# Kernel tuning notes

Hardware: AMD Instinct MI355X
Metric: run time of the kernel (lower is better)

The kernel has to match this reference:

```python
import jax, jax.numpy as jnp
import numpy as np

B, K, D = 8192, 256, 128


def setup_inputs() -> dict:
    key = jax.random.key(0)
    k1, k2 = jax.random.split(key)
    z = jax.random.normal(k1, (B, D), dtype=jnp.float32)
    centroids = jax.random.normal(k2, (K, D), dtype=jnp.float32)
    logvar = jnp.zeros((K, D), dtype=jnp.float32)
    return {"z": z, "centroids": centroids, "logvar": logvar}


def reference(z, centroids, logvar):
    # Mahalanobis (diagonal-covariance) distance of each z row to each centroid.
    # dist[b,k] = sum_d (z[b,d] - mu[k,d])^2 / var[k,d]
    diff = z[:, None, :] - centroids[None, :, :]          # (B, K, D)
    var = jnp.exp(logvar)[None, :, :]                      # (1, K, D)
    dist = jnp.sum(diff * diff / var, axis=2)              # (B, K)
    # Soft assignments: softmax over clusters of -0.5 * dist (stable softmax).
    return jax.nn.softmax(-0.5 * dist, axis=1)             # (B, K)
```

## Files before the change

kernel.cpp:

```cpp
#include <hip/hip_runtime.h>


typedef short     bf16x8  __attribute__((ext_vector_type(8)));
typedef float     f32x4   __attribute__((ext_vector_type(4)));
typedef unsigned short ushort_t;
typedef ushort_t  ushort8 __attribute__((ext_vector_type(8)));

constexpr int Bn = 8192, Kn = 256, Dn = 128;

__device__ __forceinline__ ushort_t bf16_rn(float x) {
    unsigned u = __float_as_uint(x);
    u = (u + 0x7FFFu + ((u >> 16) & 1u)) >> 16;
    return (ushort_t)u;
}
__device__ __forceinline__ float bf16f(ushort_t h) {
    return __uint_as_float(((unsigned)h) << 16);
}

__global__ __launch_bounds__(1024, 4)
void gmm_fused(const float* __restrict__ z, const float* __restrict__ cent,
               const float* __restrict__ lvar, float* __restrict__ out)
{
    __shared__ ushort_t Ah[32 * 256];
    __shared__ ushort_t Al[32 * 256];
    __shared__ float red[32][16];

    const int tid = threadIdx.x;
    const int w   = tid >> 6;
    const int l   = tid & 63;
    const int lg  = l >> 4;
    const int ll  = l & 15;
    const int b0  = blockIdx.x * 32;
    const int n0  = w * 16;

    bf16x8 Bh[8], Bl[8];
    float cpart = 0.0f;
    const size_t crow = (size_t)(n0 + ll) * Dn + lg * 4;
    #pragma unroll
    for (int kk = 0; kk < 8; ++kk) {
        const float4 cv = *reinterpret_cast<const float4*>(cent + crow + kk * 16);
        const float4 l4 = *reinterpret_cast<const float4*>(lvar + crow + kk * 16);
        const float a0 = __expf(-l4.x), a1 = __expf(-l4.y);
        const float a2 = __expf(-l4.z), a3 = __expf(-l4.w);
        const float f[8] = {a0, -2.0f * cv.x * a0, a1, -2.0f * cv.y * a1,
                            a2, -2.0f * cv.z * a2, a3, -2.0f * cv.w * a3};
        ushort8 hi8, lo8;
        #pragma unroll
        for (int j = 0; j < 8; ++j) {
            ushort_t h = bf16_rn(f[j]);
            hi8[j] = h;
            lo8[j] = bf16_rn(f[j] - bf16f(h));
        }
        Bh[kk] = (bf16x8)hi8;
        Bl[kk] = (bf16x8)lo8;
        cpart += cv.x * cv.x * a0 + cv.y * cv.y * a1 +
                 cv.z * cv.z * a2 + cv.w * cv.w * a3;
    }
    cpart += __shfl_xor(cpart, 16);
    cpart += __shfl_xor(cpart, 32);
    const float ck = cpart;

    {
        const int row = tid >> 5;
        const int dq  = tid & 31;
        const float4 v = *reinterpret_cast<const float4*>(z + (size_t)(b0 + row) * Dn + dq * 4);
        const float f[8] = {v.x * v.x, v.x, v.y * v.y, v.y,
                            v.z * v.z, v.z, v.w * v.w, v.w};
        ushort8 hi8, lo8;
        #pragma unroll
        for (int j = 0; j < 8; ++j) {
            ushort_t h = bf16_rn(f[j]);
            hi8[j] = h;
            lo8[j] = bf16_rn(f[j] - bf16f(h));
        }
        const int off = (row * 256 + dq * 8) ^ ((row & 7) << 3);
        *reinterpret_cast<ushort8*>(&Ah[off]) = hi8;
        *reinterpret_cast<ushort8*>(&Al[off]) = lo8;
    }
    __syncthreads();

    f32x4 acc0 = (f32x4){0.f, 0.f, 0.f, 0.f};
    f32x4 acc1 = (f32x4){0.f, 0.f, 0.f, 0.f};
    const int ar0 = ll * 256 + lg * 8;
    const int ar1 = ar0 + 16 * 256;
    const int sw  = (ll & 7) << 3;

    #pragma unroll
    for (int kk = 0; kk < 8; ++kk) {
        const int o = kk * 32;
        const bf16x8 a0h = *reinterpret_cast<const bf16x8*>(&Ah[(ar0 + o) ^ sw]);
        const bf16x8 a0l = *reinterpret_cast<const bf16x8*>(&Al[(ar0 + o) ^ sw]);
        const bf16x8 a1h = *reinterpret_cast<const bf16x8*>(&Ah[(ar1 + o) ^ sw]);
        const bf16x8 a1l = *reinterpret_cast<const bf16x8*>(&Al[(ar1 + o) ^ sw]);

        acc0 = __builtin_amdgcn_mfma_f32_16x16x32_bf16(a0h, Bh[kk], acc0, 0, 0, 0);
        acc1 = __builtin_amdgcn_mfma_f32_16x16x32_bf16(a1h, Bh[kk], acc1, 0, 0, 0);
        acc0 = __builtin_amdgcn_mfma_f32_16x16x32_bf16(a0h, Bl[kk], acc0, 0, 0, 0);
        acc1 = __builtin_amdgcn_mfma_f32_16x16x32_bf16(a1h, Bl[kk], acc1, 0, 0, 0);
        acc0 = __builtin_amdgcn_mfma_f32_16x16x32_bf16(a0l, Bh[kk], acc0, 0, 0, 0);
        acc1 = __builtin_amdgcn_mfma_f32_16x16x32_bf16(a1l, Bh[kk], acc1, 0, 0, 0);
    }

    float dv[2][4];
    #pragma unroll
    for (int r = 0; r < 4; ++r) { dv[0][r] = acc0[r] + ck; dv[1][r] = acc1[r] + ck; }

    #pragma unroll
    for (int mi = 0; mi < 2; ++mi)
        #pragma unroll
        for (int r = 0; r < 4; ++r) {
            float t = dv[mi][r];
            t = fminf(t, __shfl_xor(t, 1));
            t = fminf(t, __shfl_xor(t, 2));
            t = fminf(t, __shfl_xor(t, 4));
            t = fminf(t, __shfl_xor(t, 8));
            if (ll == 0) red[mi * 16 + lg * 4 + r][w] = t;
        }
    __syncthreads();

    float gm[2][4];
    #pragma unroll
    for (int mi = 0; mi < 2; ++mi)
        #pragma unroll
        for (int r = 0; r < 4; ++r) {
            const int row = mi * 16 + lg * 4 + r;
            const f32x4* rp = reinterpret_cast<const f32x4*>(&red[row][0]);
            f32x4 m4 = rp[0];
            #pragma unroll
            for (int q = 1; q < 4; ++q) {
                f32x4 v = rp[q];
                m4[0] = fminf(m4[0], v[0]); m4[1] = fminf(m4[1], v[1]);
                m4[2] = fminf(m4[2], v[2]); m4[3] = fminf(m4[3], v[3]);
            }
            gm[mi][r] = fminf(fminf(m4[0], m4[1]), fminf(m4[2], m4[3]));
        }
    __syncthreads();

    float pv[2][4];
    #pragma unroll
    for (int mi = 0; mi < 2; ++mi)
        #pragma unroll
        for (int r = 0; r < 4; ++r) {
            const float p = __expf(-0.5f * (dv[mi][r] - gm[mi][r]));
            pv[mi][r] = p;
            float s = p;
            s += __shfl_xor(s, 1);
            s += __shfl_xor(s, 2);
            s += __shfl_xor(s, 4);
            s += __shfl_xor(s, 8);
            if (ll == 0) red[mi * 16 + lg * 4 + r][w] = s;
        }
    __syncthreads();

    #pragma unroll
    for (int mi = 0; mi < 2; ++mi)
        #pragma unroll
        for (int r = 0; r < 4; ++r) {
            const int row = mi * 16 + lg * 4 + r;
            const f32x4* rp = reinterpret_cast<const f32x4*>(&red[row][0]);
            f32x4 s4 = rp[0];
            #pragma unroll
            for (int q = 1; q < 4; ++q) {
                f32x4 v = rp[q];
                s4[0] += v[0]; s4[1] += v[1]; s4[2] += v[2]; s4[3] += v[3];
            }
            const float inv = 1.0f / ((s4[0] + s4[1]) + (s4[2] + s4[3]));
            out[(size_t)(b0 + row) * Kn + n0 + ll] = pv[mi][r] * inv;
        }
}

extern "C" void kernel_launch(void* const* d_in, const int* in_sizes, int n_in,
                              void* d_out, int out_size, void* d_ws, size_t ws_size,
                              hipStream_t stream) {
    const float* z      = (const float*)d_in[0];
    const float* cent   = (const float*)d_in[1];
    const float* logvar = (const float*)d_in[2];
    float* out = (float*)d_out;
    (void)in_sizes; (void)n_in; (void)out_size; (void)d_ws; (void)ws_size;

    hipLaunchKernelGGL(gmm_fused, dim3(Bn / 32), dim3(1024), 0, stream,
                       z, cent, logvar, out);
}
```

Before: 25.35 us.

## Stream centroid prep into MFMA loop and store A tile in MFMA order

```diff
diff --git a/kernel.cpp b/kernel.cpp
--- a/kernel.cpp
+++ b/kernel.cpp
@@ -1,28 +1,38 @@
 #include <hip/hip_runtime.h>
+#include <hip/hip_bf16.h>
 
 
 typedef short     bf16x8  __attribute__((ext_vector_type(8)));
 typedef float     f32x4   __attribute__((ext_vector_type(4)));
 typedef unsigned short ushort_t;
-typedef ushort_t  ushort8 __attribute__((ext_vector_type(8)));
 
 constexpr int Bn = 8192, Kn = 256, Dn = 128;
 
-__device__ __forceinline__ ushort_t bf16_rn(float x) {
-    unsigned u = __float_as_uint(x);
-    u = (u + 0x7FFFu + ((u >> 16) & 1u)) >> 16;
-    return (ushort_t)u;
+__device__ __forceinline__ short bfbits(__hip_bfloat16 h) {
+    return __builtin_bit_cast(short, h);
 }
-__device__ __forceinline__ float bf16f(ushort_t h) {
-    return __uint_as_float(((unsigned)h) << 16);
+
+__device__ __forceinline__ void split8(const float* f, bf16x8& hi, bf16x8& lo) {
+    #pragma unroll
+    for (int p = 0; p < 4; ++p) {
+        const float2 fp = make_float2(f[2 * p], f[2 * p + 1]);
+        const __hip_bfloat162 h2 = __float22bfloat162_rn(fp);
+        hi[2 * p]     = bfbits(h2.x);
+        hi[2 * p + 1] = bfbits(h2.y);
+        const float2 rp = make_float2(fp.x - __bfloat162float(h2.x),
+                                      fp.y - __bfloat162float(h2.y));
+        const __hip_bfloat162 l2 = __float22bfloat162_rn(rp);
+        lo[2 * p]     = bfbits(l2.x);
+        lo[2 * p + 1] = bfbits(l2.y);
+    }
 }
 
 __global__ __launch_bounds__(1024, 4)
 void gmm_fused(const float* __restrict__ z, const float* __restrict__ cent,
                const float* __restrict__ lvar, float* __restrict__ out)
 {
-    __shared__ ushort_t Ah[32 * 256];
-    __shared__ ushort_t Al[32 * 256];
+    __shared__ ushort_t Ah[2 * 8 * 64 * 8];
+    __shared__ ushort_t Al[2 * 8 * 64 * 8];
     __shared__ float red[32][16];
 
     const int tid = threadIdx.x;
@@ -33,73 +43,65 @@
     const int b0  = blockIdx.x * 32;
     const int n0  = w * 16;
 
-    bf16x8 Bh[8], Bl[8];
-    float cpart = 0.0f;
-    const size_t crow = (size_t)(n0 + ll) * Dn + lg * 4;
-    #pragma unroll
-    for (int kk = 0; kk < 8; ++kk) {
-        const float4 cv = *reinterpret_cast<const float4*>(cent + crow + kk * 16);
-        const float4 l4 = *reinterpret_cast<const float4*>(lvar + crow + kk * 16);
-        const float a0 = __expf(-l4.x), a1 = __expf(-l4.y);
-        const float a2 = __expf(-l4.z), a3 = __expf(-l4.w);
-        const float f[8] = {a0, -2.0f * cv.x * a0, a1, -2.0f * cv.y * a1,
-                            a2, -2.0f * cv.z * a2, a3, -2.0f * cv.w * a3};
-        ushort8 hi8, lo8;
-        #pragma unroll
-        for (int j = 0; j < 8; ++j) {
-            ushort_t h = bf16_rn(f[j]);
-            hi8[j] = h;
-            lo8[j] = bf16_rn(f[j] - bf16f(h));
-        }
-        Bh[kk] = (bf16x8)hi8;
-        Bl[kk] = (bf16x8)lo8;
-        cpart += cv.x * cv.x * a0 + cv.y * cv.y * a1 +
-                 cv.z * cv.z * a2 + cv.w * cv.w * a3;
-    }
-    cpart += __shfl_xor(cpart, 16);
-    cpart += __shfl_xor(cpart, 32);
-    const float ck = cpart;
-
     {
-        const int row = tid >> 5;
-        const int dq  = tid & 31;
-        const float4 v = *reinterpret_cast<const float4*>(z + (size_t)(b0 + row) * Dn + dq * 4);
+        const int r   = tid >> 9;
+        const int kks = (tid >> 6) & 7;
+        const int row = r * 16 + ll;
+        const int d0  = kks * 16 + lg * 4;
+        const float4 v = *reinterpret_cast<const float4*>(
+            z + (size_t)(b0 + row) * Dn + d0);
         const float f[8] = {v.x * v.x, v.x, v.y * v.y, v.y,
                             v.z * v.z, v.z, v.w * v.w, v.w};
-        ushort8 hi8, lo8;
-        #pragma unroll
-        for (int j = 0; j < 8; ++j) {
-            ushort_t h = bf16_rn(f[j]);
-            hi8[j] = h;
-            lo8[j] = bf16_rn(f[j] - bf16f(h));
-        }
-        const int off = (row * 256 + dq * 8) ^ ((row & 7) << 3);
-        *reinterpret_cast<ushort8*>(&Ah[off]) = hi8;
-        *reinterpret_cast<ushort8*>(&Al[off]) = lo8;
+        bf16x8 hi, lo;
+        split8(f, hi, lo);
+        const int off = tid * 8;
+        *reinterpret_cast<bf16x8*>(&Ah[off]) = hi;
+        *reinterpret_cast<bf16x8*>(&Al[off]) = lo;
     }
     __syncthreads();
 
     f32x4 acc0 = (f32x4){0.f, 0.f, 0.f, 0.f};
     f32x4 acc1 = (f32x4){0.f, 0.f, 0.f, 0.f};
-    const int ar0 = ll * 256 + lg * 8;
-    const int ar1 = ar0 + 16 * 256;
-    const int sw  = (ll & 7) << 3;
+    float cpart = 0.0f;
+    const size_t crow = (size_t)(n0 + ll) * Dn + lg * 4;
+
+    float4 cv = *reinterpret_cast<const float4*>(cent + crow);
+    float4 v4 = *reinterpret_cast<const float4*>(lvar + crow);
 
     #pragma unroll
     for (int kk = 0; kk < 8; ++kk) {
-        const int o = kk * 32;
-        const bf16x8 a0h = *reinterpret_cast<const bf16x8*>(&Ah[(ar0 + o) ^ sw]);
-        const bf16x8 a0l = *reinterpret_cast<const bf16x8*>(&Al[(ar0 + o) ^ sw]);
-        const bf16x8 a1h = *reinterpret_cast<const bf16x8*>(&Ah[(ar1 + o) ^ sw]);
-        const bf16x8 a1l = *reinterpret_cast<const bf16x8*>(&Al[(ar1 + o) ^ sw]);
+        float4 ncv, nv4;
+        if (kk < 7) {
+            ncv = *reinterpret_cast<const float4*>(cent + crow + (kk + 1) * 16);
+            nv4 = *reinterpret_cast<const float4*>(lvar + crow + (kk + 1) * 16);
+        }
+        const float a0 = __expf(-v4.x), a1 = __expf(-v4.y);
+        const float a2 = __expf(-v4.z), a3 = __expf(-v4.w);
+        const float f[8] = {a0, -2.0f * cv.x * a0, a1, -2.0f * cv.y * a1,
+                            a2, -2.0f * cv.z * a2, a3, -2.0f * cv.w * a3};
+        bf16x8 Bh, Bl;
+        split8(f, Bh, Bl);
+        cpart += cv.x * cv.x * a0 + cv.y * cv.y * a1 +
+                 cv.z * cv.z * a2 + cv.w * cv.w * a3;
 
-        acc0 = __builtin_amdgcn_mfma_f32_16x16x32_bf16(a0h, Bh[kk], acc0, 0, 0, 0);
-        acc1 = __builtin_amdgcn_mfma_f32_16x16x32_bf16(a1h, Bh[kk], acc1, 0, 0, 0);
-        acc0 = __builtin_amdgcn_mfma_f32_16x16x32_bf16(a0h, Bl[kk], acc0, 0, 0, 0);
-        acc1 = __builtin_amdgcn_mfma_f32_16x16x32_bf16(a1h, Bl[kk], acc1, 0, 0, 0);
-        acc0 = __builtin_amdgcn_mfma_f32_16x16x32_bf16(a0l, Bh[kk], acc0, 0, 0, 0);
-        acc1 = __builtin_amdgcn_mfma_f32_16x16x32_bf16(a1l, Bh[kk], acc1, 0, 0, 0);
+        const int ao = kk * 512 + l * 8;
+        const bf16x8 a0h = *reinterpret_cast<const bf16x8*>(&Ah[ao]);
+        const bf16x8 a0l = *reinterpret_cast<const bf16x8*>(&Al[ao]);
+        const bf16x8 a1h = *reinterpret_cast<const bf16x8*>(&Ah[4096 + ao]);
+        const bf16x8 a1l = *reinterpret_cast<const bf16x8*>(&Al[4096 + ao]);
+
+        acc0 = __builtin_amdgcn_mfma_f32_16x16x32_bf16(a0h, Bh, acc0, 0, 0, 0);
+        acc1 = __builtin_amdgcn_mfma_f32_16x16x32_bf16(a1h, Bh, acc1, 0, 0, 0);
+        acc0 = __builtin_amdgcn_mfma_f32_16x16x32_bf16(a0h, Bl, acc0, 0, 0, 0);
+        acc1 = __builtin_amdgcn_mfma_f32_16x16x32_bf16(a1h, Bl, acc1, 0, 0, 0);
+        acc0 = __builtin_amdgcn_mfma_f32_16x16x32_bf16(a0l, Bh, acc0, 0, 0, 0);
+        acc1 = __builtin_amdgcn_mfma_f32_16x16x32_bf16(a1l, Bh, acc1, 0, 0, 0);
+
+        cv = ncv; v4 = nv4;
     }
+    cpart += __shfl_xor(cpart, 16);
+    cpart += __shfl_xor(cpart, 32);
+    const float ck = cpart;
 
     float dv[2][4];
     #pragma unroll
```

Measured after the change: 21.94 us. 13.4% less time.
